# Performance work log

Hardware: AMD Instinct MI355X
Metric: run time of the kernel (lower is better)

The kernel has to match this reference:

```python
import jax, jax.numpy as jnp
import numpy as np
from jax import lax

B, N, R, L = 16, 256, 24, 32
MEAN_STOP_TIME_S = 60.0
AVG_TRANSFER_WAIT_TIME_S = 300.0
SYMMETRIC_ROUTES = True
INF = jnp.inf


def setup_inputs() -> dict:
    key = jax.random.key(0)
    k1, k2, k3 = jax.random.split(key, 3)
    drive_times = jax.random.uniform(k1, (B, N, N), jnp.float32) * 1000.0 + 30.0
    demand = jax.random.uniform(k2, (B, N, N), jnp.float32) * 10.0
    demand = demand * (1.0 - jnp.eye(N, dtype=jnp.float32))  # no self-demand
    batch_routes = jax.random.randint(k3, (B, R, L), 0, N, dtype=jnp.int32)
    return {"drive_times": drive_times, "demand": demand, "batch_routes": batch_routes}


def _route_edges_and_legs(routes, dtm):
    # routes: [B,R,L] node ids (no -1 padding in this setup); dtm: [B,N,N]
    b = jnp.arange(B)[:, None, None]
    sf, st = routes[:, :, :-1], routes[:, :, 1:]
    leg_fwd = dtm[b, sf, st] + MEAN_STOP_TIME_S            # [B,R,L-1]
    zero = jnp.zeros((B, R, 1), dtm.dtype)
    cum_f = jnp.concatenate([zero, jnp.cumsum(leg_fwd, -1)], -1)  # [B,R,L]
    tri = jnp.triu(jnp.ones((L, L), dtype=bool), 1)
    # ride time from stop position i to position j>i along the route
    t_f = jnp.where(tri, cum_f[:, :, None, :] - cum_f[:, :, :, None], INF)
    b4 = jnp.arange(B)[:, None, None, None]
    src = jnp.broadcast_to(routes[:, :, :, None], (B, R, L, L))
    dst = jnp.broadcast_to(routes[:, :, None, :], (B, R, L, L))
    edge = jnp.full((B, N, N), INF, dtm.dtype)
    edge = edge.at[b4, src, dst].min(t_f)
    leg_rev = None
    if SYMMETRIC_ROUTES:
        leg_rev = dtm[b, st, sf] + MEAN_STOP_TIME_S        # reverse-direction legs
        cum_r = jnp.concatenate([zero, jnp.cumsum(leg_rev, -1)], -1)
        t_r = jnp.where(tri, cum_r[:, :, None, :] - cum_r[:, :, :, None], INF)
        edge = edge.at[b4, dst, src].min(t_r)              # ride from s_j back to s_i
    return edge, leg_fwd, leg_rev


def _floyd_warshall(edge):
    # batched FW, also tracking hop count of shortest paths
    idx = jnp.arange(N)
    dist = edge.at[:, idx, idx].set(0.0)
    offdiag = ~jnp.eye(N, dtype=bool)
    hops = jnp.where(jnp.isfinite(dist) & offdiag, 1.0, 0.0)

    def body(carry, k):
        d, h = carry
        dc = lax.dynamic_slice_in_dim(d, k, 1, axis=2)  # [B,N,1]
        dr = lax.dynamic_slice_in_dim(d, k, 1, axis=1)  # [B,1,N]
        hc = lax.dynamic_slice_in_dim(h, k, 1, axis=2)
        hr = lax.dynamic_slice_in_dim(h, k, 1, axis=1)
        alt = dc + dr
        better = alt < d
        return (jnp.where(better, alt, d), jnp.where(better, hc + hr, h)), None

    (dist, hops), _ = lax.scan(body, (dist, hops), idx)
    return dist, hops


def reference(drive_times, demand, batch_routes):
    edge, leg_fwd, leg_rev = _route_edges_and_legs(batch_routes, drive_times)
    dist, hops = _floyd_warshall(edge)
    nopath = jnp.isinf(dist)
    path_lens = jnp.where(nopath, 0.0, hops + 1.0)  # n nodes on path (diag -> 1)
    transfers = jnp.where(path_lens == 0.0, 0.0, path_lens - 2.0)
    trip_times = jnp.where(nopath, 0.0, dist + transfers * AVG_TRANSFER_WAIT_TIME_S)
    total_demand_time = (demand * trip_times).sum((1, 2))
    total_transfers = (demand * transfers).sum((1, 2))
    unserved_demand = jnp.where(nopath, demand, 0.0).sum((1, 2))
    total_demand = demand.sum((1, 2))
    n_disconnected = (nopath & (demand > 0)).sum((1, 2))
    buckets = [jnp.where(transfers == float(ii), demand, 0.0).sum((1, 2)) for ii in range(3)]
    d_un = jnp.where(transfers > 2.0, demand, 0.0).sum((1, 2)) + unserved_demand
    trips_at_transfers = jnp.stack(buckets + [d_un], axis=1)  # [B,4]
    total_route_time = leg_fwd.sum((1, 2))
    if SYMMETRIC_ROUTES:
        total_route_time = total_route_time + leg_rev.sum((1, 2))
    return (total_demand_time, total_route_time, trips_at_transfers,
            total_demand, unserved_demand, total_transfers, trip_times,
            n_disconnected)
```

## Files before the change

kernel.cpp:

```cpp
#include <hip/hip_runtime.h>

#define BB 16
#define NL 256
#define RR 24
#define LL 32
#define NN (NL*NL)
#define BNN (BB*NN)
#define TT 64

#define O_TDT 0
#define O_RT  16
#define O_TAT 32
#define O_TD  96
#define O_UNS 112
#define O_TTR 128
#define O_TT  144
#define O_ND  1048720

#define HSC 9.3132257461547852e-10
#define H2  1073741824.0
#define HMASK 8191

#define RIDX(r, c2) (((r)<<6) + ((((c2) ^ ((r)&31)))<<1))
#define LDD(A, r, c2) (*(double2*)&A[RIDX((r),(c2))])
#define ELEM(A, r, c) A[RIDX((r), (c)>>1) + ((c)&1)]

__global__ __launch_bounds__(1024) void k_init(double2* __restrict__ dist2, float* __restrict__ acc){
    int idx = blockIdx.x*1024 + threadIdx.x;
    double inf = __builtin_huge_val();
    double2 v = make_double2(inf, inf);
    int q = (idx*2) & (NN-1);
    int r = q % 257;
    if (r == 0)   v.x = 0.0;
    if (r == 256) v.y = 0.0;
    dist2[idx] = v;
    if (blockIdx.x == 0 && threadIdx.x < 256) acc[threadIdx.x] = 0.f;
}

__global__ void k_routes(const float* __restrict__ dtm, const int* __restrict__ routes,
                         unsigned long long* __restrict__ dist, float* __restrict__ acc){
    int br = blockIdx.x; int b = br / RR, r = br % RR;
    int lane = threadIdx.x;
    __shared__ int   s[LL];
    __shared__ float lf[LL], lr[LL], cf[LL], cr[LL];
    if (lane < LL) s[lane] = routes[(b*RR + r)*LL + lane];
    __syncthreads();
    if (lane < LL-1){
        int a0 = s[lane], a1 = s[lane+1];
        const float* dt = dtm + b*NN;
        lf[lane] = dt[a0*NL + a1] + 60.0f;
        lr[lane] = dt[a1*NL + a0] + 60.0f;
    }
    __syncthreads();
    if (lane == 0){
        float af = 0.f, ar = 0.f;
        cf[0] = 0.f; cr[0] = 0.f;
        for (int l = 0; l < LL-1; l++){
            af += lf[l]; ar += lr[l];
            cf[l+1] = af; cr[l+1] = ar;
        }
        atomicAdd(&acc[b*16 + 1], af + ar);
    }
    __syncthreads();
    for (int p = lane; p < LL*LL; p += 64){
        int i = p >> 5, j = p & 31;
        if (j > i){
            double vf = (double)(cf[j] - cf[i]) + HSC;
            double vr = (double)(cr[j] - cr[i]) + HSC;
            atomicMin(&dist[b*NN + s[i]*NL + s[j]], (unsigned long long)__double_as_longlong(vf));
            atomicMin(&dist[b*NN + s[j]*NL + s[i]], (unsigned long long)__double_as_longlong(vr));
        }
    }
}

__global__ __launch_bounds__(1024, 4) void k_fw_round(
        const double* __restrict__ src, double* __restrict__ dst, int kb){
    int b  = blockIdx.y;
    int m  = blockIdx.x;
    int ti = m >> 2, tj = m & 3;
    int t  = threadIdx.x;
    int r0 = (t >> 5) << 1;
    int c2 = t & 31;
    __shared__ double KD[4096];
    __shared__ double BD[4096];
    const double* Kg = src + b*NN + kb*TT*(NL+1);
    const double* Bg = src + b*NN + kb*TT*NL + tj*TT;
    const double* Cg = src + b*NN + ti*TT*NL + kb*TT;
    const double* Dg = src + b*NN + ti*TT*NL + tj*TT;

    double2 c0[2], d0[2];
    #pragma unroll
    for (int i = 0; i < 2; i++){
        c0[i] = *(const double2*)(Cg + (r0+i)*NL + c2*2);
        d0[i] = *(const double2*)(Dg + (r0+i)*NL + c2*2);
    }

    #pragma unroll
    for (int u = 0; u < 2; u++){
        int fid = u*1024 + t;
        int row = fid >> 5, cc = fid & 31;
        LDD(KD, row, cc) = *(const double2*)(Kg + row*NL + cc*2);
        LDD(BD, row, cc) = *(const double2*)(Bg + row*NL + cc*2);
    }
    __syncthreads();

    for (int skb = 0; skb < 4; skb++){
        int s0 = skb*16, sc2 = skb*8;
        if (t < 64){
            int i = t >> 2, jg = t & 3, rr = s0 + i, cb = sc2 + jg*2;
            double2 m0 = LDD(KD, rr, cb), m1 = LDD(KD, rr, cb+1);
            double md4[4] = {m0.x, m0.y, m1.x, m1.y};
            #pragma unroll
            for (int k = 0; k < 16; k++){
                double rd[4];
                #pragma unroll
                for (int c = 0; c < 4; c++) rd[c] = __shfl(md4[c], (k<<2)|jg);
                double cd = __shfl(md4[k&3], (i<<2)|(k>>2));
                #pragma unroll
                for (int c = 0; c < 4; c++) md4[c] = fmin(md4[c], cd + rd[c]);
            }
            LDD(KD, rr, cb)   = make_double2(md4[0], md4[1]);
            LDD(KD, rr, cb+1) = make_double2(md4[2], md4[3]);
        }
        __syncthreads();
        int rr_r = s0 + (t >> 6);
        int cc_r = t & 63;
        int rr_c = t >> 4;
        int cc_c = s0 + (t & 15);
        double sr = ELEM(KD, rr_r, cc_r);
        double sc = ELEM(KD, rr_c, cc_c);
        #pragma unroll
        for (int k = 0; k < 16; k++){
            double ar = ELEM(KD, rr_r, s0 + k);
            double br = ELEM(KD, s0 + k, cc_r);
            sr = fmin(sr, ar + br);
            double acl = ELEM(KD, rr_c, s0 + k);
            double bcl = ELEM(KD, s0 + k, cc_c);
            sc = fmin(sc, acl + bcl);
        }
        __syncthreads();
        ELEM(KD, rr_r, cc_r) = sr;
        ELEM(KD, rr_c, cc_c) = sc;
        __syncthreads();
        double2 dd0 = LDD(KD, r0, c2), dd1 = LDD(KD, r0+1, c2);
        double dd[2][2] = {{dd0.x, dd0.y}, {dd1.x, dd1.y}};
        #pragma unroll
        for (int q4 = 0; q4 < 4; q4++){
            int kr = s0 + q4*4;
            double a[2][4]; double2 bm[4];
            #pragma unroll
            for (int i = 0; i < 2; i++){
                double2 a0 = LDD(KD, r0+i, sc2+q4*2), a1 = LDD(KD, r0+i, sc2+q4*2+1);
                a[i][0]=a0.x; a[i][1]=a0.y; a[i][2]=a1.x; a[i][3]=a1.y;
            }
            #pragma unroll
            for (int q = 0; q < 4; q++) bm[q] = LDD(KD, kr+q, c2);
            #pragma unroll
            for (int q = 0; q < 4; q++)
            #pragma unroll
            for (int i = 0; i < 2; i++){
                dd[i][0] = fmin(dd[i][0], a[i][q] + bm[q].x);
                dd[i][1] = fmin(dd[i][1], a[i][q] + bm[q].y);
            }
        }
        __syncthreads();
        LDD(KD, r0,   c2) = make_double2(dd[0][0], dd[0][1]);
        LDD(KD, r0+1, c2) = make_double2(dd[1][0], dd[1][1]);
        __syncthreads();
    }

    double inf = __builtin_huge_val();
    double md[2][2] = {{inf, inf}, {inf, inf}};
    #pragma unroll 4
    for (int q4 = 0; q4 < 16; q4++){
        double a[2][4]; double2 bm[4];
        #pragma unroll
        for (int i = 0; i < 2; i++){
            double2 a0 = LDD(KD, r0+i, q4*2), a1 = LDD(KD, r0+i, q4*2+1);
            a[i][0]=a0.x; a[i][1]=a0.y; a[i][2]=a1.x; a[i][3]=a1.y;
        }
        int kr = q4*4;
        #pragma unroll
        for (int q = 0; q < 4; q++) bm[q] = LDD(BD, kr+q, c2);
        #pragma unroll
        for (int q = 0; q < 4; q++)
        #pragma unroll
        for (int i = 0; i < 2; i++){
            md[i][0] = fmin(md[i][0], a[i][q] + bm[q].x);
            md[i][1] = fmin(md[i][1], a[i][q] + bm[q].y);
        }
    }
    __syncthreads();
    LDD(BD, r0,   c2) = make_double2(md[0][0], md[0][1]);
    LDD(BD, r0+1, c2) = make_double2(md[1][0], md[1][1]);
    LDD(KD, r0,   c2) = c0[0];
    LDD(KD, r0+1, c2) = c0[1];
    __syncthreads();

    double dd[2][2] = {{d0[0].x, d0[0].y}, {d0[1].x, d0[1].y}};
    #pragma unroll 4
    for (int q4 = 0; q4 < 16; q4++){
        double a[2][4]; double2 bm[4];
        #pragma unroll
        for (int i = 0; i < 2; i++){
            double2 a0 = LDD(KD, r0+i, q4*2), a1 = LDD(KD, r0+i, q4*2+1);
            a[i][0]=a0.x; a[i][1]=a0.y; a[i][2]=a1.x; a[i][3]=a1.y;
        }
        int kr = q4*4;
        #pragma unroll
        for (int q = 0; q < 4; q++) bm[q] = LDD(BD, kr+q, c2);
        #pragma unroll
        for (int q = 0; q < 4; q++)
        #pragma unroll
        for (int i = 0; i < 2; i++){
            dd[i][0] = fmin(dd[i][0], a[i][q] + bm[q].x);
            dd[i][1] = fmin(dd[i][1], a[i][q] + bm[q].y);
        }
    }
    double* Od = dst + b*NN + ti*TT*NL + tj*TT;
    #pragma unroll
    for (int i = 0; i < 2; i++)
        *(double2*)(Od + (r0+i)*NL + c2*2) = make_double2(dd[i][0], dd[i][1]);
}

__global__ __launch_bounds__(1024) void k_epi(const double2* __restrict__ dist2,
        const float4* __restrict__ demand4, float* __restrict__ out, float* __restrict__ acc){
    int b = blockIdx.y;
    int fid = (b*NN >> 2) + blockIdx.x*1024 + threadIdx.x;
    long long q2 = (long long)fid * 2;
    double2 va = dist2[q2], vb = dist2[q2+1];
    double vs[4] = {va.x, va.y, vb.x, vb.y};
    float4 mv = demand4[fid];
    float ms[4] = {mv.x, mv.y, mv.z, mv.w};
    float s0=0,s1=0,s2=0,s3=0,s4=0,s5=0,s6=0,s7=0,s8=0;
    float tts[4];
    #pragma unroll
    for (int e = 0; e < 4; e++){
        double v = vs[e];
        bool np = !(v < 1e37);
        double vv = np ? 0.0 : v;
        int h = (int)(((long long)(vv * H2)) & (long long)HMASK);
        float d = (float)vv;
        float dm = ms[e];
        float pl = np ? 0.f : (float)(h + 1);
        float tr = (pl == 0.f) ? 0.f : pl - 2.f;
        float tt = np ? 0.f : d + tr*300.f;
        tts[e] = tt;
        s0 += dm*tt;
        s1 += dm*tr;
        s2 += np ? dm : 0.f;
        s3 += dm;
        s4 += (np && dm > 0.f) ? 1.f : 0.f;
        s5 += (tr == 0.f) ? dm : 0.f;
        s6 += (tr == 1.f) ? dm : 0.f;
        s7 += (tr == 2.f) ? dm : 0.f;
        s8 += (tr > 2.f) ? dm : 0.f;
    }
    ((float4*)(out + O_TT))[fid] = make_float4(tts[0],tts[1],tts[2],tts[3]);
    #define RED(x) { x += __shfl_down(x,32); x += __shfl_down(x,16); x += __shfl_down(x,8); \
                     x += __shfl_down(x,4);  x += __shfl_down(x,2);  x += __shfl_down(x,1); }
    RED(s0) RED(s1) RED(s2) RED(s3) RED(s4) RED(s5) RED(s6) RED(s7) RED(s8)
    __shared__ float red[16][9];
    int w = threadIdx.x >> 6;
    if ((threadIdx.x & 63) == 0){
        red[w][0]=s0; red[w][1]=s1; red[w][2]=s2; red[w][3]=s3; red[w][4]=s4;
        red[w][5]=s5; red[w][6]=s6; red[w][7]=s7; red[w][8]=s8;
    }
    __syncthreads();
    if (threadIdx.x < 9){
        float v = 0.f;
        #pragma unroll
        for (int ww = 0; ww < 16; ww++) v += red[ww][threadIdx.x];
        int slot = (threadIdx.x == 0) ? 0 : threadIdx.x + 1;
        atomicAdd(&acc[b*16 + slot], v);
    }
    __syncthreads();
    __shared__ int isLast;
    if (threadIdx.x == 0){
        unsigned prev = atomicAdd((unsigned int*)(acc + 255), 1u);
        isLast = (prev == 255u) ? 1 : 0;
    }
    __syncthreads();
    if (isLast && threadIdx.x < BB){
        int bb = threadIdx.x;
        float a[10];
        #pragma unroll
        for (int s = 0; s < 10; s++) a[s] = atomicAdd(&acc[bb*16 + s], 0.f);
        out[O_TDT + bb] = a[0];
        out[O_RT  + bb] = a[1];
        out[O_TAT + 4*bb + 0] = a[6];
        out[O_TAT + 4*bb + 1] = a[7];
        out[O_TAT + 4*bb + 2] = a[8];
        out[O_TAT + 4*bb + 3] = a[9] + a[3];
        out[O_TD  + bb] = a[4];
        out[O_UNS + bb] = a[3];
        out[O_TTR + bb] = a[2];
        out[O_ND  + bb] = a[5];
    }
}

extern "C" void kernel_launch(void* const* d_in, const int* in_sizes, int n_in,
                              void* d_out, int out_size, void* d_ws, size_t ws_size,
                              hipStream_t stream){
    (void)in_sizes; (void)n_in; (void)out_size; (void)ws_size;
    const float* dtm    = (const float*)d_in[0];
    const float* demand = (const float*)d_in[1];
    const int*   routes = (const int*)d_in[2];
    float* out   = (float*)d_out;
    double* distA = (double*)d_ws;
    double* distB = distA + BNN;
    float*  acc   = (float*)(distB + BNN);

    k_init  <<<512, 1024, 0, stream>>>((double2*)distA, acc);
    k_routes<<<BB*RR,  64, 0, stream>>>(dtm, routes, (unsigned long long*)distA, acc);
    k_fw_round<<<dim3(16,BB), 1024, 0, stream>>>(distA, distB, 0);
    k_fw_round<<<dim3(16,BB), 1024, 0, stream>>>(distB, distA, 1);
    k_fw_round<<<dim3(16,BB), 1024, 0, stream>>>(distA, distB, 2);
    k_fw_round<<<dim3(16,BB), 1024, 0, stream>>>(distB, distA, 3);
    k_epi<<<dim3(16,BB), 1024, 0, stream>>>((const double2*)distA,
                                            (const float4*)demand, out, acc);
}
```

Baseline: 246.6 us.

## Use 4x4 register tiles per thread in blocked Floyd-Warshall round kernel

Drops the FW round kernel from 1024 to 256 threads per block, each computing a 4x4 tile of the 64x64 block instead of 2x2. The row/column panel update is also changed so each thread updates four contiguous elements with the A operands preloaded into registers. The aim is to cut LDS traffic per min-plus operation through more register reuse. The cost is fewer waves per block, fewer threads to hide latency in the serial diagonal phase, and higher register pressure.

Result: slower. 256.5 us (+4.0%).

```diff
diff --git a/kernel.cpp b/kernel.cpp
--- a/kernel.cpp
+++ b/kernel.cpp
@@ -23,7 +23,6 @@
 
 #define RIDX(r, c2) (((r)<<6) + ((((c2) ^ ((r)&31)))<<1))
 #define LDD(A, r, c2) (*(double2*)&A[RIDX((r),(c2))])
-#define ELEM(A, r, c) A[RIDX((r), (c)>>1) + ((c)&1)]
 
 __global__ __launch_bounds__(1024) void k_init(double2* __restrict__ dist2, float* __restrict__ acc){
     int idx = blockIdx.x*1024 + threadIdx.x;
@@ -73,14 +72,15 @@
     }
 }
 
-__global__ __launch_bounds__(1024, 4) void k_fw_round(
+__global__ __launch_bounds__(256, 1) void k_fw_round(
         const double* __restrict__ src, double* __restrict__ dst, int kb){
     int b  = blockIdx.y;
     int m  = blockIdx.x;
     int ti = m >> 2, tj = m & 3;
     int t  = threadIdx.x;
-    int r0 = (t >> 5) << 1;
-    int c2 = t & 31;
+    int r0 = (t >> 4) << 2;
+    int c2 = (t & 15) << 1;
+    int c4 = (t & 15) << 2;
     __shared__ double KD[4096];
     __shared__ double BD[4096];
     const double* Kg = src + b*NN + kb*TT*(NL+1);
@@ -88,16 +88,18 @@
     const double* Cg = src + b*NN + ti*TT*NL + kb*TT;
     const double* Dg = src + b*NN + ti*TT*NL + tj*TT;
 
-    double2 c0[2], d0[2];
-    #pragma unroll
-    for (int i = 0; i < 2; i++){
-        c0[i] = *(const double2*)(Cg + (r0+i)*NL + c2*2);
-        d0[i] = *(const double2*)(Dg + (r0+i)*NL + c2*2);
-    }
-
-    #pragma unroll
-    for (int u = 0; u < 2; u++){
-        int fid = u*1024 + t;
+    double2 c0[4][2], d0[4][2];
+    #pragma unroll
+    for (int i = 0; i < 4; i++){
+        c0[i][0] = *(const double2*)(Cg + (r0+i)*NL + c4);
+        c0[i][1] = *(const double2*)(Cg + (r0+i)*NL + c4 + 2);
+        d0[i][0] = *(const double2*)(Dg + (r0+i)*NL + c4);
+        d0[i][1] = *(const double2*)(Dg + (r0+i)*NL + c4 + 2);
+    }
+
+    #pragma unroll
+    for (int u = 0; u < 8; u++){
+        int fid = u*256 + t;
         int row = fid >> 5, cc = fid & 31;
         LDD(KD, row, cc) = *(const double2*)(Kg + row*NL + cc*2);
         LDD(BD, row, cc) = *(const double2*)(Bg + row*NL + cc*2);
@@ -123,104 +125,151 @@
             LDD(KD, rr, cb+1) = make_double2(md4[2], md4[3]);
         }
         __syncthreads();
-        int rr_r = s0 + (t >> 6);
-        int cc_r = t & 63;
-        int rr_c = t >> 4;
-        int cc_c = s0 + (t & 15);
-        double sr = ELEM(KD, rr_r, cc_r);
-        double sc = ELEM(KD, rr_c, cc_c);
+        int rs_r  = s0 + (t >> 4);
+        int rs_c2 = (t & 15) << 1;
+        int cs_r  = t >> 2;
+        int cs_c2 = sc2 + ((t & 3) << 1);
+        double rs[4], cs[4], ar[16], ac[16];
+        {
+            double2 v0 = LDD(KD, rs_r, rs_c2), v1 = LDD(KD, rs_r, rs_c2+1);
+            rs[0]=v0.x; rs[1]=v0.y; rs[2]=v1.x; rs[3]=v1.y;
+            double2 w0 = LDD(KD, cs_r, cs_c2), w1 = LDD(KD, cs_r, cs_c2+1);
+            cs[0]=w0.x; cs[1]=w0.y; cs[2]=w1.x; cs[3]=w1.y;
+            #pragma unroll
+            for (int c = 0; c < 8; c++){
+                double2 av = LDD(KD, rs_r, sc2 + c);
+                ar[2*c] = av.x; ar[2*c+1] = av.y;
+                double2 aw = LDD(KD, cs_r, sc2 + c);
+                ac[2*c] = aw.x; ac[2*c+1] = aw.y;
+            }
+        }
         #pragma unroll
         for (int k = 0; k < 16; k++){
-            double ar = ELEM(KD, rr_r, s0 + k);
-            double br = ELEM(KD, s0 + k, cc_r);
-            sr = fmin(sr, ar + br);
-            double acl = ELEM(KD, rr_c, s0 + k);
-            double bcl = ELEM(KD, s0 + k, cc_c);
-            sc = fmin(sc, acl + bcl);
-        }
-        __syncthreads();
-        ELEM(KD, rr_r, cc_r) = sr;
-        ELEM(KD, rr_c, cc_c) = sc;
-        __syncthreads();
-        double2 dd0 = LDD(KD, r0, c2), dd1 = LDD(KD, r0+1, c2);
-        double dd[2][2] = {{dd0.x, dd0.y}, {dd1.x, dd1.y}};
+            double2 b0 = LDD(KD, s0+k, rs_c2), b1 = LDD(KD, s0+k, rs_c2+1);
+            rs[0] = fmin(rs[0], ar[k] + b0.x);
+            rs[1] = fmin(rs[1], ar[k] + b0.y);
+            rs[2] = fmin(rs[2], ar[k] + b1.x);
+            rs[3] = fmin(rs[3], ar[k] + b1.y);
+            double2 e0 = LDD(KD, s0+k, cs_c2), e1 = LDD(KD, s0+k, cs_c2+1);
+            cs[0] = fmin(cs[0], ac[k] + e0.x);
+            cs[1] = fmin(cs[1], ac[k] + e0.y);
+            cs[2] = fmin(cs[2], ac[k] + e1.x);
+            cs[3] = fmin(cs[3], ac[k] + e1.y);
+        }
+        __syncthreads();
+        LDD(KD, rs_r, rs_c2)   = make_double2(rs[0], rs[1]);
+        LDD(KD, rs_r, rs_c2+1) = make_double2(rs[2], rs[3]);
+        LDD(KD, cs_r, cs_c2)   = make_double2(cs[0], cs[1]);
+        LDD(KD, cs_r, cs_c2+1) = make_double2(cs[2], cs[3]);
+        __syncthreads();
+        double dd[4][4];
+        #pragma unroll
+        for (int i = 0; i < 4; i++){
+            double2 v0 = LDD(KD, r0+i, c2), v1 = LDD(KD, r0+i, c2+1);
+            dd[i][0]=v0.x; dd[i][1]=v0.y; dd[i][2]=v1.x; dd[i][3]=v1.y;
+        }
         #pragma unroll
         for (int q4 = 0; q4 < 4; q4++){
             int kr = s0 + q4*4;
-            double a[2][4]; double2 bm[4];
-            #pragma unroll
-            for (int i = 0; i < 2; i++){
+            double a[4][4], bm[4][4];
+            #pragma unroll
+            for (int i = 0; i < 4; i++){
                 double2 a0 = LDD(KD, r0+i, sc2+q4*2), a1 = LDD(KD, r0+i, sc2+q4*2+1);
                 a[i][0]=a0.x; a[i][1]=a0.y; a[i][2]=a1.x; a[i][3]=a1.y;
             }
             #pragma unroll
-            for (int q = 0; q < 4; q++) bm[q] = LDD(KD, kr+q, c2);
+            for (int q = 0; q < 4; q++){
+                double2 b0 = LDD(KD, kr+q, c2), b1 = LDD(KD, kr+q, c2+1);
+                bm[q][0]=b0.x; bm[q][1]=b0.y; bm[q][2]=b1.x; bm[q][3]=b1.y;
+            }
             #pragma unroll
             for (int q = 0; q < 4; q++)
             #pragma unroll
-            for (int i = 0; i < 2; i++){
-                dd[i][0] = fmin(dd[i][0], a[i][q] + bm[q].x);
-                dd[i][1] = fmin(dd[i][1], a[i][q] + bm[q].y);
-            }
-        }
-        __syncthreads();
-        LDD(KD, r0,   c2) = make_double2(dd[0][0], dd[0][1]);
-        LDD(KD, r0+1, c2) = make_double2(dd[1][0], dd[1][1]);
+            for (int i = 0; i < 4; i++)
+            #pragma unroll
+            for (int j = 0; j < 4; j++)
+                dd[i][j] = fmin(dd[i][j], a[i][q] + bm[q][j]);
+        }
+        __syncthreads();
+        #pragma unroll
+        for (int i = 0; i < 4; i++){
+            LDD(KD, r0+i, c2)   = make_double2(dd[i][0], dd[i][1]);
+            LDD(KD, r0+i, c2+1) = make_double2(dd[i][2], dd[i][3]);
+        }
         __syncthreads();
     }
 
     double inf = __builtin_huge_val();
-    double md[2][2] = {{inf, inf}, {inf, inf}};
+    double md[4][4];
+    #pragma unroll
+    for (int i = 0; i < 4; i++)
+    #pragma unroll
+    for (int j = 0; j < 4; j++) md[i][j] = inf;
     #pragma unroll 4
     for (int q4 = 0; q4 < 16; q4++){
-        double a[2][4]; double2 bm[4];
-        #pragma unroll
-        for (int i = 0; i < 2; i++){
+        double a[4][4], bm[4][4];
+        #pragma unroll
+        for (int i = 0; i < 4; i++){
             double2 a0 = LDD(KD, r0+i, q4*2), a1 = LDD(KD, r0+i, q4*2+1);
             a[i][0]=a0.x; a[i][1]=a0.y; a[i][2]=a1.x; a[i][3]=a1.y;
         }
         int kr = q4*4;
         #pragma unroll
-        for (int q = 0; q < 4; q++) bm[q] = LDD(BD, kr+q, c2);
+        for (int q = 0; q < 4; q++){
+            double2 b0 = LDD(BD, kr+q, c2), b1 = LDD(BD, kr+q, c2+1);
+            bm[q][0]=b0.x; bm[q][1]=b0.y; bm[q][2]=b1.x; bm[q][3]=b1.y;
+        }
         #pragma unroll
         for (int q = 0; q < 4; q++)
         #pragma unroll
-        for (int i = 0; i < 2; i++){
-            md[i][0] = fmin(md[i][0], a[i][q] + bm[q].x);
-            md[i][1] = fmin(md[i][1], a[i][q] + bm[q].y);
-        }
-    }
-    __syncthreads();
-    LDD(BD, r0,   c2) = make_double2(md[0][0], md[0][1]);
-    LDD(BD, r0+1, c2) = make_double2(md[1][0], md[1][1]);
-    LDD(KD, r0,   c2) = c0[0];
-    LDD(KD, r0+1, c2) = c0[1];
-    __syncthreads();
-
-    double dd[2][2] = {{d0[0].x, d0[0].y}, {d0[1].x, d0[1].y}};
+        for (int i = 0; i < 4; i++)
+        #pragma unroll
+        for (int j = 0; j < 4; j++)
+            md[i][j] = fmin(md[i][j], a[i][q] + bm[q][j]);
+    }
+    __syncthreads();
+    #pragma unroll
+    for (int i = 0; i < 4; i++){
+        LDD(BD, r0+i, c2)   = make_double2(md[i][0], md[i][1]);
+        LDD(BD, r0+i, c2+1) = make_double2(md[i][2], md[i][3]);
+        LDD(KD, r0+i, c2)   = c0[i][0];
+        LDD(KD, r0+i, c2+1) = c0[i][1];
+    }
+    __syncthreads();
+
+    double dd[4][4];
+    #pragma unroll
+    for (int i = 0; i < 4; i++){
+        dd[i][0]=d0[i][0].x; dd[i][1]=d0[i][0].y; dd[i][2]=d0[i][1].x; dd[i][3]=d0[i][1].y;
+    }
     #pragma unroll 4
     for (int q4 = 0; q4 < 16; q4++){
-        double a[2][4]; double2 bm[4];
-        #pragma unroll
-        for (int i = 0; i < 2; i++){
+        double a[4][4], bm[4][4];
+        #pragma unroll
+        for (int i = 0; i < 4; i++){
             double2 a0 = LDD(KD, r0+i, q4*2), a1 = LDD(KD, r0+i, q4*2+1);
             a[i][0]=a0.x; a[i][1]=a0.y; a[i][2]=a1.x; a[i][3]=a1.y;
         }
         int kr = q4*4;
         #pragma unroll
-        for (int q = 0; q < 4; q++) bm[q] = LDD(BD, kr+q, c2);
+        for (int q = 0; q < 4; q++){
+            double2 b0 = LDD(BD, kr+q, c2), b1 = LDD(BD, kr+q, c2+1);
+            bm[q][0]=b0.x; bm[q][1]=b0.y; bm[q][2]=b1.x; bm[q][3]=b1.y;
+        }
         #pragma unroll
         for (int q = 0; q < 4; q++)
         #pragma unroll
-        for (int i = 0; i < 2; i++){
-            dd[i][0] = fmin(dd[i][0], a[i][q] + bm[q].x);
-            dd[i][1] = fmin(dd[i][1], a[i][q] + bm[q].y);
-        }
+        for (int i = 0; i < 4; i++)
+        #pragma unroll
+        for (int j = 0; j < 4; j++)
+            dd[i][j] = fmin(dd[i][j], a[i][q] + bm[q][j]);
     }
     double* Od = dst + b*NN + ti*TT*NL + tj*TT;
     #pragma unroll
-    for (int i = 0; i < 2; i++)
-        *(double2*)(Od + (r0+i)*NL + c2*2) = make_double2(dd[i][0], dd[i][1]);
+    for (int i = 0; i < 4; i++){
+        *(double2*)(Od + (r0+i)*NL + c4)     = make_double2(dd[i][0], dd[i][1]);
+        *(double2*)(Od + (r0+i)*NL + c4 + 2) = make_double2(dd[i][2], dd[i][3]);
+    }
 }
 
 __global__ __launch_bounds__(1024) void k_epi(const double2* __restrict__ dist2,
@@ -313,10 +362,10 @@
 
     k_init  <<<512, 1024, 0, stream>>>((double2*)distA, acc);
     k_routes<<<BB*RR,  64, 0, stream>>>(dtm, routes, (unsigned long long*)distA, acc);
-    k_fw_round<<<dim3(16,BB), 1024, 0, stream>>>(distA, distB, 0);
-    k_fw_round<<<dim3(16,BB), 1024, 0, stream>>>(distB, distA, 1);
-    k_fw_round<<<dim3(16,BB), 1024, 0, stream>>>(distA, distB, 2);
-    k_fw_round<<<dim3(16,BB), 1024, 0, stream>>>(distB, distA, 3);
+    k_fw_round<<<dim3(16,BB), 256, 0, stream>>>(distA, distB, 0);
+    k_fw_round<<<dim3(16,BB), 256, 0, stream>>>(distB, distA, 1);
+    k_fw_round<<<dim3(16,BB), 256, 0, stream>>>(distA, distB, 2);
+    k_fw_round<<<dim3(16,BB), 256, 0, stream>>>(distB, distA, 3);
     k_epi<<<dim3(16,BB), 1024, 0, stream>>>((const double2*)distA,
                                             (const float4*)demand, out, acc);
 }
```

## Split blocked Floyd-Warshall into diag, panel and inner kernels in place

Applied to the files above, without the earlier changes.

Replaces the single per-round kernel, in which every one of the 16 blocks recomputed the diagonal tile and its panels redundantly, with the standard three-phase blocked FW: one diagonal kernel, one panel kernel and one inner-tile kernel, all updating one buffer in place. The min-plus multiply now uses 256 threads, each computing a 4x4 register tile, instead of 1024 threads with 2x2 each. This removes the redundant diagonal and panel work and the double buffer. In exchange it launches three times as many kernels with serial dependencies and runs far fewer threads per block, which can lower occupancy.

New measurement: 263.5 us. +6.9%, slower.

```diff
diff --git a/kernel.cpp b/kernel.cpp
--- a/kernel.cpp
+++ b/kernel.cpp
@@ -73,37 +73,20 @@
     }
 }
 
-__global__ __launch_bounds__(1024, 4) void k_fw_round(
-        const double* __restrict__ src, double* __restrict__ dst, int kb){
-    int b  = blockIdx.y;
-    int m  = blockIdx.x;
-    int ti = m >> 2, tj = m & 3;
-    int t  = threadIdx.x;
+__global__ __launch_bounds__(1024, 4) void k_diag(double* __restrict__ D, int kb){
+    int b = blockIdx.x;
+    int t = threadIdx.x;
     int r0 = (t >> 5) << 1;
     int c2 = t & 31;
     __shared__ double KD[4096];
-    __shared__ double BD[4096];
-    const double* Kg = src + b*NN + kb*TT*(NL+1);
-    const double* Bg = src + b*NN + kb*TT*NL + tj*TT;
-    const double* Cg = src + b*NN + ti*TT*NL + kb*TT;
-    const double* Dg = src + b*NN + ti*TT*NL + tj*TT;
-
-    double2 c0[2], d0[2];
-    #pragma unroll
-    for (int i = 0; i < 2; i++){
-        c0[i] = *(const double2*)(Cg + (r0+i)*NL + c2*2);
-        d0[i] = *(const double2*)(Dg + (r0+i)*NL + c2*2);
-    }
-
+    double* Kg = D + b*NN + kb*TT*(NL+1);
     #pragma unroll
     for (int u = 0; u < 2; u++){
         int fid = u*1024 + t;
         int row = fid >> 5, cc = fid & 31;
         LDD(KD, row, cc) = *(const double2*)(Kg + row*NL + cc*2);
-        LDD(BD, row, cc) = *(const double2*)(Bg + row*NL + cc*2);
-    }
-    __syncthreads();
-
+    }
+    __syncthreads();
     for (int skb = 0; skb < 4; skb++){
         int s0 = skb*16, sc2 = skb*8;
         if (t < 64){
@@ -168,59 +151,88 @@
         LDD(KD, r0+1, c2) = make_double2(dd[1][0], dd[1][1]);
         __syncthreads();
     }
-
-    double inf = __builtin_huge_val();
-    double md[2][2] = {{inf, inf}, {inf, inf}};
+    #pragma unroll
+    for (int u = 0; u < 2; u++){
+        int fid = u*1024 + t;
+        int row = fid >> 5, cc = fid & 31;
+        *(double2*)(Kg + row*NL + cc*2) = LDD(KD, row, cc);
+    }
+}
+
+static __device__ __forceinline__ void mul64(double* XD, double* YD,
+        const double* __restrict__ Xg, const double* __restrict__ Yg,
+        double* __restrict__ Og, int initSel){
+    int t = threadIdx.x;
+    int r0 = (t >> 4) << 2;
+    int cA = t & 15, cB = cA + 16;
+    #pragma unroll
+    for (int u = 0; u < 8; u++){
+        int fid = u*256 + t;
+        int row = fid >> 5, cc = fid & 31;
+        LDD(XD, row, cc) = *(const double2*)(Xg + row*NL + cc*2);
+        LDD(YD, row, cc) = *(const double2*)(Yg + row*NL + cc*2);
+    }
+    __syncthreads();
+    double dd[4][4];
+    #pragma unroll
+    for (int i = 0; i < 4; i++){
+        double2 v0, v1;
+        if (initSel == 1){ v0 = LDD(XD, r0+i, cA); v1 = LDD(XD, r0+i, cB); }
+        else if (initSel == 2){ v0 = LDD(YD, r0+i, cA); v1 = LDD(YD, r0+i, cB); }
+        else { v0 = *(const double2*)(Og + (r0+i)*NL + 2*cA);
+               v1 = *(const double2*)(Og + (r0+i)*NL + 2*cB); }
+        dd[i][0]=v0.x; dd[i][1]=v0.y; dd[i][2]=v1.x; dd[i][3]=v1.y;
+    }
     #pragma unroll 4
     for (int q4 = 0; q4 < 16; q4++){
-        double a[2][4]; double2 bm[4];
-        #pragma unroll
-        for (int i = 0; i < 2; i++){
-            double2 a0 = LDD(KD, r0+i, q4*2), a1 = LDD(KD, r0+i, q4*2+1);
+        int kr = q4*4, kc = q4*2;
+        double a[4][4], bm[4][4];
+        #pragma unroll
+        for (int i = 0; i < 4; i++){
+            double2 a0 = LDD(XD, r0+i, kc), a1 = LDD(XD, r0+i, kc+1);
             a[i][0]=a0.x; a[i][1]=a0.y; a[i][2]=a1.x; a[i][3]=a1.y;
         }
-        int kr = q4*4;
-        #pragma unroll
-        for (int q = 0; q < 4; q++) bm[q] = LDD(BD, kr+q, c2);
+        #pragma unroll
+        for (int q = 0; q < 4; q++){
+            double2 b0 = LDD(YD, kr+q, cA), b1 = LDD(YD, kr+q, cB);
+            bm[q][0]=b0.x; bm[q][1]=b0.y; bm[q][2]=b1.x; bm[q][3]=b1.y;
+        }
         #pragma unroll
         for (int q = 0; q < 4; q++)
         #pragma unroll
-        for (int i = 0; i < 2; i++){
-            md[i][0] = fmin(md[i][0], a[i][q] + bm[q].x);
-            md[i][1] = fmin(md[i][1], a[i][q] + bm[q].y);
-        }
-    }
-    __syncthreads();
-    LDD(BD, r0,   c2) = make_double2(md[0][0], md[0][1]);
-    LDD(BD, r0+1, c2) = make_double2(md[1][0], md[1][1]);
-    LDD(KD, r0,   c2) = c0[0];
-    LDD(KD, r0+1, c2) = c0[1];
-    __syncthreads();
-
-    double dd[2][2] = {{d0[0].x, d0[0].y}, {d0[1].x, d0[1].y}};
-    #pragma unroll 4
-    for (int q4 = 0; q4 < 16; q4++){
-        double a[2][4]; double2 bm[4];
-        #pragma unroll
-        for (int i = 0; i < 2; i++){
-            double2 a0 = LDD(KD, r0+i, q4*2), a1 = LDD(KD, r0+i, q4*2+1);
-            a[i][0]=a0.x; a[i][1]=a0.y; a[i][2]=a1.x; a[i][3]=a1.y;
-        }
-        int kr = q4*4;
-        #pragma unroll
-        for (int q = 0; q < 4; q++) bm[q] = LDD(BD, kr+q, c2);
-        #pragma unroll
-        for (int q = 0; q < 4; q++)
-        #pragma unroll
-        for (int i = 0; i < 2; i++){
-            dd[i][0] = fmin(dd[i][0], a[i][q] + bm[q].x);
-            dd[i][1] = fmin(dd[i][1], a[i][q] + bm[q].y);
-        }
-    }
-    double* Od = dst + b*NN + ti*TT*NL + tj*TT;
-    #pragma unroll
-    for (int i = 0; i < 2; i++)
-        *(double2*)(Od + (r0+i)*NL + c2*2) = make_double2(dd[i][0], dd[i][1]);
+        for (int i = 0; i < 4; i++)
+        #pragma unroll
+        for (int j = 0; j < 4; j++)
+            dd[i][j] = fmin(dd[i][j], a[i][q] + bm[q][j]);
+    }
+    #pragma unroll
+    for (int i = 0; i < 4; i++){
+        *(double2*)(Og + (r0+i)*NL + 2*cA) = make_double2(dd[i][0], dd[i][1]);
+        *(double2*)(Og + (r0+i)*NL + 2*cB) = make_double2(dd[i][2], dd[i][3]);
+    }
+}
+
+__global__ __launch_bounds__(256, 1) void k_panel(double* __restrict__ D, int kb){
+    int b = blockIdx.y, m = blockIdx.x;
+    int jj = m % 3; int other = jj + (jj >= kb);
+    __shared__ double XD[4096], YD[4096];
+    double* diag = D + b*NN + kb*TT*(NL+1);
+    if (m < 3){
+        double* Yt = D + b*NN + kb*TT*NL + other*TT;
+        mul64(XD, YD, diag, Yt, Yt, 2);
+    } else {
+        double* Xt = D + b*NN + other*TT*NL + kb*TT;
+        mul64(XD, YD, Xt, diag, Xt, 1);
+    }
+}
+
+__global__ __launch_bounds__(256, 1) void k_inner(double* __restrict__ D, int kb){
+    int b = blockIdx.y, m = blockIdx.x;
+    int i2 = m / 3, j2 = m % 3;
+    int i = i2 + (i2 >= kb), j = j2 + (j2 >= kb);
+    __shared__ double XD[4096], YD[4096];
+    mul64(XD, YD, D + b*NN + i*TT*NL + kb*TT, D + b*NN + kb*TT*NL + j*TT,
+          D + b*NN + i*TT*NL + j*TT, 0);
 }
 
 __global__ __launch_bounds__(1024) void k_epi(const double2* __restrict__ dist2,
@@ -308,15 +320,15 @@
     const int*   routes = (const int*)d_in[2];
     float* out   = (float*)d_out;
     double* distA = (double*)d_ws;
-    double* distB = distA + BNN;
-    float*  acc   = (float*)(distB + BNN);
+    float*  acc   = (float*)(distA + BNN);
 
     k_init  <<<512, 1024, 0, stream>>>((double2*)distA, acc);
     k_routes<<<BB*RR,  64, 0, stream>>>(dtm, routes, (unsigned long long*)distA, acc);
-    k_fw_round<<<dim3(16,BB), 1024, 0, stream>>>(distA, distB, 0);
-    k_fw_round<<<dim3(16,BB), 1024, 0, stream>>>(distB, distA, 1);
-    k_fw_round<<<dim3(16,BB), 1024, 0, stream>>>(distA, distB, 2);
-    k_fw_round<<<dim3(16,BB), 1024, 0, stream>>>(distB, distA, 3);
+    for (int kb = 0; kb < 4; kb++){
+        k_diag <<<BB,          1024, 0, stream>>>(distA, kb);
+        k_panel<<<dim3(6,BB),   256, 0, stream>>>(distA, kb);
+        k_inner<<<dim3(9,BB),   256, 0, stream>>>(distA, kb);
+    }
     k_epi<<<dim3(16,BB), 1024, 0, stream>>>((const double2*)distA,
                                             (const float4*)demand, out, acc);
 }
```
